# Performance work log

Hardware: AMD Instinct MI355X
Metric: run time of the kernel (lower is better)

The kernel has to match this reference:

```python
import jax, jax.numpy as jnp
import numpy as np

B, T, H, I, OUT = 128, 1440, 512, 2, 1
TAU, ALPHA = 6.0, 0.1


def setup_inputs() -> dict:
    key = jax.random.key(0)
    ks = jax.random.split(key, 8)
    xs = jax.random.normal(ks[0], (B, T), dtype=jnp.float32)
    # sparse 0/1 observation mask (channel 2); channel 1 unused by forward
    mask = (jax.random.uniform(ks[1], (B, T)) < 0.05).astype(jnp.float32)
    inp = jnp.stack([xs, jnp.zeros((B, T), jnp.float32), mask], axis=1)[..., None]  # [B,3,T,1]
    s = 1.0 / np.sqrt(H)
    u = lambda k, shp: jax.random.uniform(k, shp, minval=-s, maxval=s, dtype=jnp.float32)
    return {
        "input": inp,
        "w_ih": u(ks[2], (3 * H, I)),
        "w_hh": u(ks[3], (3 * H, H)),
        "b_ih": u(ks[4], (3 * H,)),
        "b_hh": u(ks[5], (3 * H,)),
        "w_fc": u(ks[6], (OUT, H)),
        "b_fc": u(ks[7], (OUT,)),
    }


def belief_fill(x, mask, half_tau):
    # Vectorized equivalent of the per-batch / per-observed-index Python loop:
    # each position takes the value of the next observed index if within half_tau
    # else the previous observed index if within half_tau, else stays unchanged.
    Ts = x.shape[1]
    t = jnp.arange(Ts)[None, :]
    obs = mask == 1
    p = jax.lax.cummax(jnp.where(obs, t, -1), axis=1)                       # prev observed idx or -1
    n = jax.lax.cummin(jnp.where(obs, t, Ts)[:, ::-1], axis=1)[:, ::-1]      # next observed idx or Ts
    xp = jnp.take_along_axis(x, jnp.clip(p, 0, Ts - 1), axis=1)
    xn = jnp.take_along_axis(x, jnp.clip(n, 0, Ts - 1), axis=1)
    use_n = (n < Ts) & (t >= n - half_tau)
    use_p = (p >= 0) & (t <= p + half_tau)
    return jnp.where(use_n, xn, jnp.where(use_p, xp, x))


def _forward(inp, w_ih, w_hh, b_ih, b_hh, w_fc, b_fc):
    xs = inp[:, 0, :, 0]      # [B,T]
    masks = inp[:, 2, :, 0]   # [B,T]
    xs = jnp.where(jnp.isnan(xs), -1.0, xs)
    # tau update: old_weight is ones(3H, I)
    grads = jnp.mean(w_ih - 1.0)
    tau_new = TAU + grads * ALPHA
    trigger = (tau_new >= 1.0) & (tau_new != TAU)
    half_tau = jnp.round(tau_new / 2.0)
    xs = jnp.where(trigger, belief_fill(xs, masks, half_tau), xs)
    gru_in = jnp.stack((xs, masks), axis=2)  # [B,T,2]
    # precompute input projections once (the only input-dependent GEMM)
    gi = jnp.einsum('bti,gi->btg', gru_in, w_ih) + b_ih  # [B,T,3H]

    def step(h, gi_t):
        gh = h @ w_hh.T + b_hh
        r = jax.nn.sigmoid(gi_t[:, :H] + gh[:, :H])
        z = jax.nn.sigmoid(gi_t[:, H:2 * H] + gh[:, H:2 * H])
        ng = jnp.tanh(gi_t[:, 2 * H:] + r * gh[:, 2 * H:])
        h = (1.0 - z) * ng + z * h
        return h, None

    h0 = jnp.zeros((inp.shape[0], H), gi.dtype)
    h_last, _ = jax.lax.scan(step, h0, jnp.swapaxes(gi, 0, 1))
    return h_last @ w_fc.T + b_fc  # [B, OUT]


def reference(input, w_ih, w_hh, b_ih, b_hh, w_fc, b_fc):
    return _forward(input, w_ih, w_hh, b_ih, b_hh, w_fc, b_fc)
```

## Files before the change

kernel.cpp:

```cpp
#include <hip/hip_runtime.h>
#include <math.h>

#define BN   128
#define TN   1440
#define HN   512
#define GBn  8
#define BSn  16
#define GCn  32
#define HCn  16
#define WST  536

using f16 = _Float16;
typedef f16   f16x8 __attribute__((ext_vector_type(8)));
typedef float f32x4 __attribute__((ext_vector_type(4)));
typedef unsigned int       uint32;
typedef unsigned long long u64;

#define OFF_SCAL 1024
#define OFF_HBUF 2048
#define OFF_XSF  (2048 + 2 * BN * HN * 4)

__global__ void k_prep(const float* __restrict__ w_ih, float* __restrict__ scal) {
    __shared__ float ssum[4];
    float s = 0.0f;
    for (int i = threadIdx.x; i < 3 * HN * 2; i += 256) s += w_ih[i];
    for (int o = 32; o >= 1; o >>= 1) s += __shfl_down(s, o, 64);
    if ((threadIdx.x & 63) == 0) ssum[threadIdx.x >> 6] = s;
    __syncthreads();
    if (threadIdx.x == 0) {
        float tot = ssum[0] + ssum[1] + ssum[2] + ssum[3];
        float grads = tot / 3072.0f - 1.0f;
        float tau_new = 6.0f + grads * 0.1f;
        bool trig = (tau_new >= 1.0f) && (tau_new != 6.0f);
        scal[0] = rintf(tau_new * 0.5f);
        scal[1] = trig ? 1.0f : 0.0f;
    }
}

__global__ void k_fill(const float* __restrict__ inp, const float* __restrict__ scal,
                       float* __restrict__ xsf) {
    const int b = blockIdx.x;
    const int lane = threadIdx.x;
    const float ht = scal[0];
    const bool trig = scal[1] != 0.0f;
    const float* xrow = inp + (size_t)b * 3 * TN;
    const float* mrow = xrow + 2 * TN;
    const int CH = 23;
    const int start = lane * CH;

    if (!trig) {
        for (int i = 0; i < CH; ++i) {
            int t = start + i;
            if (t < TN) { float x = xrow[t]; if (x != x) x = -1.0f; xsf[(size_t)b * TN + t] = x; }
        }
        return;
    }
    int pm = -1;
#pragma unroll
    for (int i = 0; i < CH; ++i) { int t = start + i; if (t < TN && mrow[t] == 1.0f) pm = t; }
    int incl = pm;
    for (int o = 1; o < 64; o <<= 1) { int v = __shfl_up(incl, o, 64); if (lane >= o) incl = max(incl, v); }
    int pexcl = __shfl_up(incl, 1, 64); if (lane == 0) pexcl = -1;
    int nm = TN;
#pragma unroll
    for (int i = CH - 1; i >= 0; --i) { int t = start + i; if (t < TN && mrow[t] == 1.0f) nm = t; }
    int incl2 = nm;
    for (int o = 1; o < 64; o <<= 1) { int v = __shfl_down(incl2, o, 64); if (lane + o < 64) incl2 = min(incl2, v); }
    int nexcl = __shfl_down(incl2, 1, 64); if (lane == 63) nexcl = TN;
    int narr[23];
    int runn = nexcl;
#pragma unroll
    for (int i = CH - 1; i >= 0; --i) {
        int t = start + i;
        if (t < TN) { if (mrow[t] == 1.0f) runn = t; narr[i] = runn; } else narr[i] = TN;
    }
    int runp = pexcl;
#pragma unroll
    for (int i = 0; i < CH; ++i) {
        int t = start + i;
        if (t >= TN) break;
        float x = xrow[t]; if (x != x) x = -1.0f;
        if (mrow[t] == 1.0f) runp = t;
        int pv = runp, nv = narr[i];
        int pc = min(max(pv, 0), TN - 1), nc = min(max(nv, 0), TN - 1);
        float xp = xrow[pc]; if (xp != xp) xp = -1.0f;
        float xn = xrow[nc]; if (xn != xn) xn = -1.0f;
        bool use_n = (nv < TN) && ((float)t >= (float)nv - ht);
        bool use_p = (pv >= 0) && ((float)t <= (float)pv + ht);
        float o = use_n ? xn : (use_p ? xp : x);
        xsf[(size_t)b * TN + t] = o;
    }
}

__global__ __launch_bounds__(256, 1) void k_gru(
    const float* __restrict__ inp, const float* __restrict__ w_ih,
    const float* __restrict__ w_hh, const float* __restrict__ b_ih,
    const float* __restrict__ b_hh, const float* __restrict__ w_fc,
    const float* __restrict__ b_fc, const float* __restrict__ xsf,
    uint32* __restrict__ hbufP, int* __restrict__ flags, float* __restrict__ out) {
    __shared__ __align__(16) f16 sHhi[BSn * WST];
    __shared__ __align__(16) f16 sHlo[BSn * WST];
    __shared__ float sGh[3][BSn][HCn + 1];
    __shared__ float sWi0[48], sWi1[48], sBias[48];

    const int tid = threadIdx.x;
    const int gb = blockIdx.x & 7;
    const int gc = blockIdx.x >> 3;
    const int lane = tid & 63;
    const int wv   = tid >> 6;
    const int bs   = tid >> 4;
    const int j    = tid & 15;
    const int bglob = gb * BSn + bs;
    const int pcol  = gc * HCn + j;
    const int frow = lane & 15;
    const int kgrp = lane >> 4;

    if (tid < 48) {
        int gate = tid >> 4, jj = tid & 15;
        int grow = gate * HN + gc * HCn + jj;
        sWi0[tid]  = w_ih[grow * 2 + 0];
        sWi1[tid]  = w_ih[grow * 2 + 1];
        sBias[tid] = b_ih[grow] + b_hh[grow];
    }

    f16x8 bfh[16], bfl[16];
    if (wv < 3) {
        const float* wrow = w_hh + (size_t)(wv * HN + gc * HCn + frow) * HN;
#pragma unroll
        for (int c = 0; c < 16; ++c) {
            const int k0 = (c * 4 + kgrp) * 8;
#pragma unroll
            for (int u = 0; u < 8; ++u) {
                float w = wrow[k0 + u];
                f16 hi = (f16)w;
                bfh[c][u] = hi;
                bfl[c][u] = (f16)((w - (float)hi) * 2048.0f);
            }
        }
    }
    __syncthreads();

    int* myflags = flags + gb * GCn;
    const f16x8* pAhi = (const f16x8*)(sHhi + frow * WST);
    const f16x8* pAlo = (const f16x8*)(sHlo + frow * WST);
    float h = 0.0f;

    for (int t = 0; t < TN; ++t) {
        float xsv = xsf[(size_t)bglob * TN + t];
        float mkv = inp[((size_t)bglob * 3 + 2) * TN + t];
        if (lane < GCn) {
            while (__hip_atomic_load(&myflags[lane], __ATOMIC_RELAXED, __HIP_MEMORY_SCOPE_AGENT) < t) {}
        }
        {
            const uint32* src = hbufP + ((size_t)(t & 1) * BN + gb * BSn) * HN;
            u64 hv[16];
#pragma unroll
            for (int i = 0; i < 16; ++i)
                hv[i] = __hip_atomic_load((const u64*)(src + (size_t)i * HN) + tid,
                                          __ATOMIC_RELAXED, __HIP_MEMORY_SCOPE_AGENT);
#pragma unroll
            for (int i = 0; i < 16; ++i) {
                uint32 d0 = (uint32)hv[i], d1 = (uint32)(hv[i] >> 32);
                ((uint32*)(sHhi + i * WST))[tid] = __builtin_amdgcn_perm(d1, d0, 0x05040100u);
                ((uint32*)(sHlo + i * WST))[tid] = __builtin_amdgcn_perm(d1, d0, 0x07060302u);
            }
        }
        __syncthreads();
        if (wv < 3) {
            f32x4 acch = {0.f, 0.f, 0.f, 0.f}, accl = {0.f, 0.f, 0.f, 0.f};
#pragma unroll
            for (int c = 0; c < 16; ++c) {
                f16x8 ah = pAhi[c * 4 + kgrp];
                f16x8 al = pAlo[c * 4 + kgrp];
                acch = __builtin_amdgcn_mfma_f32_16x16x32_f16(ah, bfh[c], acch, 0, 0, 0);
                accl = __builtin_amdgcn_mfma_f32_16x16x32_f16(ah, bfl[c], accl, 0, 0, 0);
                accl = __builtin_amdgcn_mfma_f32_16x16x32_f16(al, bfh[c], accl, 0, 0, 0);
            }
#pragma unroll
            for (int r = 0; r < 4; ++r)
                sGh[wv][kgrp * 4 + r][frow] = acch[r] + accl[r] * (1.0f / 2048.0f);
        }
        __syncthreads();
        {
            float ghr = sGh[0][bs][j], ghz = sGh[1][bs][j], ghn = sGh[2][bs][j];
            float gir = xsv * sWi0[j]      + mkv * sWi1[j]      + sBias[j];
            float giz = xsv * sWi0[16 + j] + mkv * sWi1[16 + j] + sBias[16 + j];
            float gin = xsv * sWi0[32 + j] + mkv * sWi1[32 + j] + sBias[32 + j];
            float rg = 1.0f / (1.0f + __expf(-(gir + ghr)));
            float zg = 1.0f / (1.0f + __expf(-(giz + ghz)));
            float ng = tanhf(gin + rg * ghn);
            h = (1.0f - zg) * ng + zg * h;
            f16 hi = (f16)h;
            f16 lo = (f16)((h - (float)hi) * 2048.0f);
            uint32 pk = (uint32)__builtin_bit_cast(unsigned short, hi)
                      | ((uint32)__builtin_bit_cast(unsigned short, lo) << 16);
            __hip_atomic_store(&hbufP[((size_t)((t + 1) & 1) * BN + bglob) * HN + pcol], pk,
                               __ATOMIC_RELAXED, __HIP_MEMORY_SCOPE_AGENT);
        }
        __syncthreads();
        if (tid == 0)
            __hip_atomic_store(&myflags[gc], t + 1, __ATOMIC_RELAXED, __HIP_MEMORY_SCOPE_AGENT);
    }
    float part = h * w_fc[pcol];
#pragma unroll
    for (int o = 1; o < 16; o <<= 1) part += __shfl_xor(part, o, 64);
    if (j == 0) {
        if (gc == 0) part += b_fc[0];
        atomicAdd(&out[bglob], part);
    }
}

extern "C" void kernel_launch(void* const* d_in, const int* in_sizes, int n_in,
                              void* d_out, int out_size, void* d_ws, size_t ws_size,
                              hipStream_t stream) {
    const float* inp  = (const float*)d_in[0];
    const float* w_ih = (const float*)d_in[1];
    const float* w_hh = (const float*)d_in[2];
    const float* b_ih = (const float*)d_in[3];
    const float* b_hh = (const float*)d_in[4];
    const float* w_fc = (const float*)d_in[5];
    const float* b_fc = (const float*)d_in[6];
    float* out = (float*)d_out;
    char* ws = (char*)d_ws;
    int*    flags = (int*)ws;
    float*  scal  = (float*)(ws + OFF_SCAL);
    uint32* hbufP = (uint32*)(ws + OFF_HBUF);
    float*  xsf   = (float*)(ws + OFF_XSF);

    hipMemsetAsync(ws, 0, OFF_HBUF + BN * HN * 4, stream);
    hipMemsetAsync(d_out, 0, BN * sizeof(float), stream);
    k_prep<<<1, 256, 0, stream>>>(w_ih, scal);
    k_fill<<<BN, 64, 0, stream>>>(inp, scal, xsf);
    k_gru<<<GBn * GCn, 256, 0, stream>>>(inp, w_ih, w_hh, b_ih, b_hh, w_fc, b_fc,
                                         xsf, hbufP, flags, out);
}
```

Before: 3.912 ms.

## Replace per-block step flags with timestep-tagged hidden state words

The hidden-state exchange buffer now holds 64-bit words that pack the hi/lo f16 payload with the timestep number. Consumers spin on the data itself instead of separate per-block flags. This removes the trailing block barrier and the flag store/poll round trip each step, cutting inter-block synchronisation latency. In exchange the buffer doubles in size, each step reads twice the bytes, and polling retries individual words, which may raise memory traffic.

```diff
diff --git a/kernel.cpp b/kernel.cpp
--- a/kernel.cpp
+++ b/kernel.cpp
@@ -18,7 +18,7 @@
 
 #define OFF_SCAL 1024
 #define OFF_HBUF 2048
-#define OFF_XSF  (2048 + 2 * BN * HN * 4)
+#define OFF_XSF  (OFF_HBUF + 2 * BN * HN * 8)
 
 __global__ void k_prep(const float* __restrict__ w_ih, float* __restrict__ scal) {
     __shared__ float ssum[4];
@@ -97,7 +97,7 @@
     const float* __restrict__ w_hh, const float* __restrict__ b_ih,
     const float* __restrict__ b_hh, const float* __restrict__ w_fc,
     const float* __restrict__ b_fc, const float* __restrict__ xsf,
-    uint32* __restrict__ hbufP, int* __restrict__ flags, float* __restrict__ out) {
+    u64* __restrict__ hbuf, float* __restrict__ out) {
     __shared__ __align__(16) f16 sHhi[BSn * WST];
     __shared__ __align__(16) f16 sHlo[BSn * WST];
     __shared__ float sGh[3][BSn][HCn + 1];
@@ -140,32 +140,52 @@
     }
     __syncthreads();
 
-    int* myflags = flags + gb * GCn;
     const f16x8* pAhi = (const f16x8*)(sHhi + frow * WST);
     const f16x8* pAlo = (const f16x8*)(sHlo + frow * WST);
+    unsigned short* sHhiU = (unsigned short*)sHhi;
+    unsigned short* sHloU = (unsigned short*)sHlo;
     float h = 0.0f;
 
     for (int t = 0; t < TN; ++t) {
         float xsv = xsf[(size_t)bglob * TN + t];
         float mkv = inp[((size_t)bglob * 3 + 2) * TN + t];
+        const u64* rbase = hbuf + ((size_t)(t & 1) * BN + gb * BSn) * HN;
+
         if (lane < GCn) {
-            while (__hip_atomic_load(&myflags[lane], __ATOMIC_RELAXED, __HIP_MEMORY_SCOPE_AGENT) < t) {}
-        }
-        {
-            const uint32* src = hbufP + ((size_t)(t & 1) * BN + gb * BSn) * HN;
-            u64 hv[16];
-#pragma unroll
-            for (int i = 0; i < 16; ++i)
-                hv[i] = __hip_atomic_load((const u64*)(src + (size_t)i * HN) + tid,
-                                          __ATOMIC_RELAXED, __HIP_MEMORY_SCOPE_AGENT);
-#pragma unroll
-            for (int i = 0; i < 16; ++i) {
-                uint32 d0 = (uint32)hv[i], d1 = (uint32)(hv[i] >> 32);
-                ((uint32*)(sHhi + i * WST))[tid] = __builtin_amdgcn_perm(d1, d0, 0x05040100u);
-                ((uint32*)(sHlo + i * WST))[tid] = __builtin_amdgcn_perm(d1, d0, 0x07060302u);
-            }
+            const u64* s = rbase + 15 * HN + lane * HCn + (HCn - 1);
+            while ((uint32)(__hip_atomic_load(s, __ATOMIC_RELAXED, __HIP_MEMORY_SCOPE_AGENT) >> 32)
+                   != (uint32)t)
+                __builtin_amdgcn_s_sleep(1);
+        }
+
+        u64 hv[32];
+#pragma unroll
+        for (int k = 0; k < 32; ++k)
+            hv[k] = __hip_atomic_load(rbase + k * 256 + tid,
+                                      __ATOMIC_RELAXED, __HIP_MEMORY_SCOPE_AGENT);
+        while (true) {
+            int bad = 0;
+#pragma unroll
+            for (int k = 0; k < 32; ++k) bad |= ((uint32)(hv[k] >> 32) != (uint32)t);
+            if (!__any(bad)) break;
+#pragma unroll
+            for (int k = 0; k < 32; ++k)
+                if ((uint32)(hv[k] >> 32) != (uint32)t)
+                    hv[k] = __hip_atomic_load(rbase + k * 256 + tid,
+                                              __ATOMIC_RELAXED, __HIP_MEMORY_SCOPE_AGENT);
+            __builtin_amdgcn_s_sleep(1);
+        }
+
+#pragma unroll
+        for (int k = 0; k < 32; ++k) {
+            const int r = k >> 1;
+            const int c = ((k & 1) << 8) + tid;
+            uint32 pay = (uint32)hv[k];
+            sHhiU[r * WST + c] = (unsigned short)(pay & 0xffffu);
+            sHloU[r * WST + c] = (unsigned short)(pay >> 16);
         }
         __syncthreads();
+
         if (wv < 3) {
             f32x4 acch = {0.f, 0.f, 0.f, 0.f}, accl = {0.f, 0.f, 0.f, 0.f};
 #pragma unroll
@@ -181,6 +201,7 @@
                 sGh[wv][kgrp * 4 + r][frow] = acch[r] + accl[r] * (1.0f / 2048.0f);
         }
         __syncthreads();
+
         {
             float ghr = sGh[0][bs][j], ghz = sGh[1][bs][j], ghn = sGh[2][bs][j];
             float gir = xsv * sWi0[j]      + mkv * sWi1[j]      + sBias[j];
@@ -194,13 +215,12 @@
             f16 lo = (f16)((h - (float)hi) * 2048.0f);
             uint32 pk = (uint32)__builtin_bit_cast(unsigned short, hi)
                       | ((uint32)__builtin_bit_cast(unsigned short, lo) << 16);
-            __hip_atomic_store(&hbufP[((size_t)((t + 1) & 1) * BN + bglob) * HN + pcol], pk,
+            u64 val = (u64)pk | ((u64)(uint32)(t + 1) << 32);
+            __hip_atomic_store(&hbuf[((size_t)((t + 1) & 1) * BN + bglob) * HN + pcol], val,
                                __ATOMIC_RELAXED, __HIP_MEMORY_SCOPE_AGENT);
         }
-        __syncthreads();
-        if (tid == 0)
-            __hip_atomic_store(&myflags[gc], t + 1, __ATOMIC_RELAXED, __HIP_MEMORY_SCOPE_AGENT);
-    }
+    }
+
     float part = h * w_fc[pcol];
 #pragma unroll
     for (int o = 1; o < 16; o <<= 1) part += __shfl_xor(part, o, 64);
@@ -222,15 +242,14 @@
     const float* b_fc = (const float*)d_in[6];
     float* out = (float*)d_out;
     char* ws = (char*)d_ws;
-    int*    flags = (int*)ws;
-    float*  scal  = (float*)(ws + OFF_SCAL);
-    uint32* hbufP = (uint32*)(ws + OFF_HBUF);
-    float*  xsf   = (float*)(ws + OFF_XSF);
-
-    hipMemsetAsync(ws, 0, OFF_HBUF + BN * HN * 4, stream);
+    float* scal = (float*)(ws + OFF_SCAL);
+    u64*   hbuf = (u64*)(ws + OFF_HBUF);
+    float* xsf  = (float*)(ws + OFF_XSF);
+
+    hipMemsetAsync(ws, 0, OFF_HBUF + 2 * BN * HN * 8, stream);
     hipMemsetAsync(d_out, 0, BN * sizeof(float), stream);
     k_prep<<<1, 256, 0, stream>>>(w_ih, scal);
     k_fill<<<BN, 64, 0, stream>>>(inp, scal, xsf);
     k_gru<<<GBn * GCn, 256, 0, stream>>>(inp, w_ih, w_hh, b_ih, b_hh, w_fc, b_fc,
-                                         xsf, hbufP, flags, out);
-}
+                                         xsf, hbuf, out);
+}
```

After: 5.841 ms. 49.3% more time.

## Tag hidden-state words with step index and pad per-block flags

Applied to the files above, without the earlier changes.

Each hidden-state element is now stored as a 64-bit word holding the packed hi/lo f16 pair plus the step number. Consumers re-poll any element whose tag does not match the expected step, so the end-of-step barrier no longer has to wait for global stores to drain before the flag is published. Per-block progress flags are padded to separate cache lines to reduce contention while spinning. In exchange, each step moves twice as many bytes of hidden state and adds per-element tag checks, and the flag wait is kept as well.

```diff
diff --git a/kernel.cpp b/kernel.cpp
--- a/kernel.cpp
+++ b/kernel.cpp
@@ -9,6 +9,7 @@
 #define GCn  32
 #define HCn  16
 #define WST  536
+#define FLSTR 32
 
 using f16 = _Float16;
 typedef f16   f16x8 __attribute__((ext_vector_type(8)));
@@ -16,9 +17,9 @@
 typedef unsigned int       uint32;
 typedef unsigned long long u64;
 
-#define OFF_SCAL 1024
-#define OFF_HBUF 2048
-#define OFF_XSF  (2048 + 2 * BN * HN * 4)
+#define OFF_SCAL 32768
+#define OFF_HBUF 33792
+#define OFF_XSF  (OFF_HBUF + 2 * BN * HN * 8)
 
 __global__ void k_prep(const float* __restrict__ w_ih, float* __restrict__ scal) {
     __shared__ float ssum[4];
@@ -97,7 +98,7 @@
     const float* __restrict__ w_hh, const float* __restrict__ b_ih,
     const float* __restrict__ b_hh, const float* __restrict__ w_fc,
     const float* __restrict__ b_fc, const float* __restrict__ xsf,
-    uint32* __restrict__ hbufP, int* __restrict__ flags, float* __restrict__ out) {
+    u64* __restrict__ hbuf, int* __restrict__ flags, float* __restrict__ out) {
     __shared__ __align__(16) f16 sHhi[BSn * WST];
     __shared__ __align__(16) f16 sHlo[BSn * WST];
     __shared__ float sGh[3][BSn][HCn + 1];
@@ -140,7 +141,7 @@
     }
     __syncthreads();
 
-    int* myflags = flags + gb * GCn;
+    int* myflags = flags + gb * GCn * FLSTR;
     const f16x8* pAhi = (const f16x8*)(sHhi + frow * WST);
     const f16x8* pAlo = (const f16x8*)(sHlo + frow * WST);
     float h = 0.0f;
@@ -148,22 +149,36 @@
     for (int t = 0; t < TN; ++t) {
         float xsv = xsf[(size_t)bglob * TN + t];
         float mkv = inp[((size_t)bglob * 3 + 2) * TN + t];
+        const u64* src = hbuf + ((size_t)(t & 1) * BN + gb * BSn) * HN;
+
         if (lane < GCn) {
-            while (__hip_atomic_load(&myflags[lane], __ATOMIC_RELAXED, __HIP_MEMORY_SCOPE_AGENT) < t) {}
-        }
-        {
-            const uint32* src = hbufP + ((size_t)(t & 1) * BN + gb * BSn) * HN;
-            u64 hv[16];
-#pragma unroll
-            for (int i = 0; i < 16; ++i)
-                hv[i] = __hip_atomic_load((const u64*)(src + (size_t)i * HN) + tid,
+            while (__hip_atomic_load(&myflags[lane * FLSTR], __ATOMIC_RELAXED,
+                                     __HIP_MEMORY_SCOPE_AGENT) < t) {}
+        }
+
+        u64 hA[16], hB[16];
+#pragma unroll
+        for (int i = 0; i < 16; ++i) {
+            hA[i] = __hip_atomic_load(src + (size_t)i * HN + 2 * tid,
+                                      __ATOMIC_RELAXED, __HIP_MEMORY_SCOPE_AGENT);
+            hB[i] = __hip_atomic_load(src + (size_t)i * HN + 2 * tid + 1,
+                                      __ATOMIC_RELAXED, __HIP_MEMORY_SCOPE_AGENT);
+        }
+#pragma unroll
+        for (int i = 0; i < 16; ++i) {
+            while ((uint32)(hA[i] >> 32) != (uint32)t)
+                hA[i] = __hip_atomic_load(src + (size_t)i * HN + 2 * tid,
                                           __ATOMIC_RELAXED, __HIP_MEMORY_SCOPE_AGENT);
-#pragma unroll
-            for (int i = 0; i < 16; ++i) {
-                uint32 d0 = (uint32)hv[i], d1 = (uint32)(hv[i] >> 32);
-                ((uint32*)(sHhi + i * WST))[tid] = __builtin_amdgcn_perm(d1, d0, 0x05040100u);
-                ((uint32*)(sHlo + i * WST))[tid] = __builtin_amdgcn_perm(d1, d0, 0x07060302u);
-            }
+            while ((uint32)(hB[i] >> 32) != (uint32)t)
+                hB[i] = __hip_atomic_load(src + (size_t)i * HN + 2 * tid + 1,
+                                          __ATOMIC_RELAXED, __HIP_MEMORY_SCOPE_AGENT);
+        }
+
+#pragma unroll
+        for (int i = 0; i < 16; ++i) {
+            uint32 d0 = (uint32)hA[i], d1 = (uint32)hB[i];
+            ((uint32*)(sHhi + i * WST))[tid] = __builtin_amdgcn_perm(d1, d0, 0x05040100u);
+            ((uint32*)(sHlo + i * WST))[tid] = __builtin_amdgcn_perm(d1, d0, 0x07060302u);
         }
         __syncthreads();
         if (wv < 3) {
@@ -194,12 +209,16 @@
             f16 lo = (f16)((h - (float)hi) * 2048.0f);
             uint32 pk = (uint32)__builtin_bit_cast(unsigned short, hi)
                       | ((uint32)__builtin_bit_cast(unsigned short, lo) << 16);
-            __hip_atomic_store(&hbufP[((size_t)((t + 1) & 1) * BN + bglob) * HN + pcol], pk,
+            u64 val = (u64)pk | ((u64)(uint32)(t + 1) << 32);
+            __hip_atomic_store(&hbuf[((size_t)((t + 1) & 1) * BN + bglob) * HN + pcol], val,
                                __ATOMIC_RELAXED, __HIP_MEMORY_SCOPE_AGENT);
         }
-        __syncthreads();
+        asm volatile("s_waitcnt lgkmcnt(0)" ::: "memory");
+        __builtin_amdgcn_s_barrier();
+        asm volatile("" ::: "memory");
         if (tid == 0)
-            __hip_atomic_store(&myflags[gc], t + 1, __ATOMIC_RELAXED, __HIP_MEMORY_SCOPE_AGENT);
+            __hip_atomic_store(&myflags[gc * FLSTR], t + 1, __ATOMIC_RELAXED,
+                               __HIP_MEMORY_SCOPE_AGENT);
     }
     float part = h * w_fc[pcol];
 #pragma unroll
@@ -224,13 +243,13 @@
     char* ws = (char*)d_ws;
     int*    flags = (int*)ws;
     float*  scal  = (float*)(ws + OFF_SCAL);
-    uint32* hbufP = (uint32*)(ws + OFF_HBUF);
+    u64*    hbuf  = (u64*)(ws + OFF_HBUF);
     float*  xsf   = (float*)(ws + OFF_XSF);
 
-    hipMemsetAsync(ws, 0, OFF_HBUF + BN * HN * 4, stream);
+    hipMemsetAsync(ws, 0, OFF_HBUF + 2 * BN * HN * 8, stream);
     hipMemsetAsync(d_out, 0, BN * sizeof(float), stream);
     k_prep<<<1, 256, 0, stream>>>(w_ih, scal);
     k_fill<<<BN, 64, 0, stream>>>(inp, scal, xsf);
     k_gru<<<GBn * GCn, 256, 0, stream>>>(inp, w_ih, w_hh, b_ih, b_hh, w_fc, b_fc,
-                                         xsf, hbufP, flags, out);
-}
+                                         xsf, hbuf, flags, out);
+}
```

Measured after the change: 6.060 ms. +54.9%, slower.

## Split recurrent GEMV K-dimension across all four waves and use fast gate math

Applied to the files above, without the earlier changes.

Before, three waves each ran the full K=512 reduction for one gate while the fourth wave sat idle. Now each of the four waves handles a quarter of K for all three gates, and the partial sums are reduced through shared memory. The per-step serial MFMA chain per wave shrinks from 48 to 36 instructions and all waves do work, which shortens the latency-bound recurrence step. It also swaps tanhf and the divisions for __expf/__fdividef forms, which is cheaper but slightly less accurate and adds LDS traffic for the partial sums.

```diff
diff --git a/kernel.cpp b/kernel.cpp
--- a/kernel.cpp
+++ b/kernel.cpp
@@ -100,7 +100,7 @@
     uint32* __restrict__ hbufP, int* __restrict__ flags, float* __restrict__ out) {
     __shared__ __align__(16) f16 sHhi[BSn * WST];
     __shared__ __align__(16) f16 sHlo[BSn * WST];
-    __shared__ float sGh[3][BSn][HCn + 1];
+    __shared__ float sPart[3][4][BSn][HCn + 1];
     __shared__ float sWi0[48], sWi1[48], sBias[48];
 
     const int tid = threadIdx.x;
@@ -123,18 +123,19 @@
         sBias[tid] = b_ih[grow] + b_hh[grow];
     }
 
-    f16x8 bfh[16], bfl[16];
-    if (wv < 3) {
-        const float* wrow = w_hh + (size_t)(wv * HN + gc * HCn + frow) * HN;
-#pragma unroll
-        for (int c = 0; c < 16; ++c) {
-            const int k0 = (c * 4 + kgrp) * 8;
+    f16x8 bfh[3][4], bfl[3][4];
+#pragma unroll
+    for (int g = 0; g < 3; ++g) {
+        const float* wrow = w_hh + (size_t)(g * HN + gc * HCn + frow) * HN;
+#pragma unroll
+        for (int kc = 0; kc < 4; ++kc) {
+            const int k0 = 128 * wv + 32 * kc + 8 * kgrp;
 #pragma unroll
             for (int u = 0; u < 8; ++u) {
                 float w = wrow[k0 + u];
                 f16 hi = (f16)w;
-                bfh[c][u] = hi;
-                bfl[c][u] = (f16)((w - (float)hi) * 2048.0f);
+                bfh[g][kc][u] = hi;
+                bfl[g][kc][u] = (f16)((w - (float)hi) * 2048.0f);
             }
         }
     }
@@ -166,29 +167,41 @@
             }
         }
         __syncthreads();
-        if (wv < 3) {
-            f32x4 acch = {0.f, 0.f, 0.f, 0.f}, accl = {0.f, 0.f, 0.f, 0.f};
-#pragma unroll
-            for (int c = 0; c < 16; ++c) {
-                f16x8 ah = pAhi[c * 4 + kgrp];
-                f16x8 al = pAlo[c * 4 + kgrp];
-                acch = __builtin_amdgcn_mfma_f32_16x16x32_f16(ah, bfh[c], acch, 0, 0, 0);
-                accl = __builtin_amdgcn_mfma_f32_16x16x32_f16(ah, bfl[c], accl, 0, 0, 0);
-                accl = __builtin_amdgcn_mfma_f32_16x16x32_f16(al, bfh[c], accl, 0, 0, 0);
+        {
+            f32x4 acch[3] = {{0.f,0.f,0.f,0.f},{0.f,0.f,0.f,0.f},{0.f,0.f,0.f,0.f}};
+            f32x4 accl[3] = {{0.f,0.f,0.f,0.f},{0.f,0.f,0.f,0.f},{0.f,0.f,0.f,0.f}};
+#pragma unroll
+            for (int kc = 0; kc < 4; ++kc) {
+                f16x8 ah = pAhi[16 * wv + kc * 4 + kgrp];
+                f16x8 al = pAlo[16 * wv + kc * 4 + kgrp];
+#pragma unroll
+                for (int g = 0; g < 3; ++g) {
+                    acch[g] = __builtin_amdgcn_mfma_f32_16x16x32_f16(ah, bfh[g][kc], acch[g], 0, 0, 0);
+                    accl[g] = __builtin_amdgcn_mfma_f32_16x16x32_f16(ah, bfl[g][kc], accl[g], 0, 0, 0);
+                    accl[g] = __builtin_amdgcn_mfma_f32_16x16x32_f16(al, bfh[g][kc], accl[g], 0, 0, 0);
+                }
             }
 #pragma unroll
-            for (int r = 0; r < 4; ++r)
-                sGh[wv][kgrp * 4 + r][frow] = acch[r] + accl[r] * (1.0f / 2048.0f);
+            for (int g = 0; g < 3; ++g)
+#pragma unroll
+                for (int r = 0; r < 4; ++r)
+                    sPart[g][wv][kgrp * 4 + r][frow] = acch[g][r] + accl[g][r] * (1.0f / 2048.0f);
         }
         __syncthreads();
         {
-            float ghr = sGh[0][bs][j], ghz = sGh[1][bs][j], ghn = sGh[2][bs][j];
+            float ghr = sPart[0][0][bs][j] + sPart[0][1][bs][j]
+                      + sPart[0][2][bs][j] + sPart[0][3][bs][j];
+            float ghz = sPart[1][0][bs][j] + sPart[1][1][bs][j]
+                      + sPart[1][2][bs][j] + sPart[1][3][bs][j];
+            float ghn = sPart[2][0][bs][j] + sPart[2][1][bs][j]
+                      + sPart[2][2][bs][j] + sPart[2][3][bs][j];
             float gir = xsv * sWi0[j]      + mkv * sWi1[j]      + sBias[j];
             float giz = xsv * sWi0[16 + j] + mkv * sWi1[16 + j] + sBias[16 + j];
             float gin = xsv * sWi0[32 + j] + mkv * sWi1[32 + j] + sBias[32 + j];
-            float rg = 1.0f / (1.0f + __expf(-(gir + ghr)));
-            float zg = 1.0f / (1.0f + __expf(-(giz + ghz)));
-            float ng = tanhf(gin + rg * ghn);
+            float rg = __fdividef(1.0f, 1.0f + __expf(-(gir + ghr)));
+            float zg = __fdividef(1.0f, 1.0f + __expf(-(giz + ghz)));
+            float xt = gin + rg * ghn;
+            float ng = __fdividef(2.0f, 1.0f + __expf(-2.0f * xt)) - 1.0f;
             h = (1.0f - zg) * ng + zg * h;
             f16 hi = (f16)h;
             f16 lo = (f16)((h - (float)hi) * 2048.0f);
```

Result: faster. 3.691 ms (median of 2 runs) (-5.6%).
